# Kernel optimization log

Hardware: AMD Instinct MI355X
Metric: run time of the kernel (lower is better)

The kernel has to match this reference:

```python
import jax, jax.numpy as jnp
import numpy as np

N_NODES = 100000
N_EDGES = 3200000
IN_DIM = 128
HID = 64
OUT_DIM = 1


def gcn_conv(x, src, dst, W, b, n_nodes):
    # PyG GCNConv: h = X W; out = D^{-1/2} (A+I) D^{-1/2} h + b
    # (src, dst already include self-loops)
    h = x @ W  # [N, F_out]
    ones = jnp.ones(src.shape[0], dtype=x.dtype)
    deg = jax.ops.segment_sum(ones, dst, num_segments=n_nodes)  # in-degree with self-loops
    dinv = jnp.where(deg > 0, jax.lax.rsqrt(deg), 0.0)
    norm = dinv[src] * dinv[dst]  # [E]
    msg = h[src] * norm[:, None]  # [E, F_out] gather + scale
    agg = jax.ops.segment_sum(msg, dst, num_segments=n_nodes)  # scatter-add
    return agg + b


def setup_inputs() -> dict:
    key = jax.random.key(0)
    k = jax.random.split(key, 8)
    x = jax.random.normal(k[0], (N_NODES, IN_DIM), dtype=jnp.float32)
    edge_index = jax.random.randint(k[1], (2, N_EDGES), 0, N_NODES, dtype=jnp.int32)
    # Glorot-ish init for weights
    W1 = jax.random.normal(k[2], (IN_DIM, HID), dtype=jnp.float32) / np.sqrt(IN_DIM)
    b1 = jnp.zeros((HID,), dtype=jnp.float32)
    W2 = jax.random.normal(k[3], (HID, HID), dtype=jnp.float32) / np.sqrt(HID)
    b2 = jnp.zeros((HID,), dtype=jnp.float32)
    Wfc = jax.random.normal(k[4], (HID, OUT_DIM), dtype=jnp.float32) / np.sqrt(HID)
    bfc = jnp.zeros((OUT_DIM,), dtype=jnp.float32)
    return {"x": x, "edge_index": edge_index, "W1": W1, "b1": b1,
            "W2": W2, "b2": b2, "Wfc": Wfc, "bfc": bfc}


def reference(x, edge_index, W1, b1, W2, b2, Wfc, bfc):
    n = x.shape[0]
    loops = jnp.arange(n, dtype=edge_index.dtype)
    src = jnp.concatenate([edge_index[0], loops])
    dst = jnp.concatenate([edge_index[1], loops])
    h = jax.nn.relu(gcn_conv(x, src, dst, W1, b1, n))
    # dropout p=0.2 is identity in eval mode
    h = jax.nn.relu(gcn_conv(h, src, dst, W2, b2, n))
    out = h @ Wfc + bfc
    return jax.nn.sigmoid(out)
```

## Files before the change

### kernel.cpp

```cpp
#include <hip/hip_runtime.h>

#define INDIM 128
#define HIDD 64
#define BSHIFT 6
#define BNODES 64
#define BCAP 4096
#define MAXBUCK 2048
#define CHUNK 8192
#define ATHREADS 512
#define BPT (MAXBUCK / ATHREADS)

typedef float f32x2 __attribute__((ext_vector_type(2)));
typedef uint4 __attribute__((aligned(4))) uint4a;

__device__ inline unsigned short f2bf(float f) {
    unsigned u = __float_as_uint(f);
    return (unsigned short)((u + 0x7fff + ((u >> 16) & 1)) >> 16);
}
__device__ inline float bflo(unsigned v) { return __uint_as_float(v << 16); }


__global__ void k_zero(int* __restrict__ p, int n) {
    int i = blockIdx.x * blockDim.x + threadIdx.x;
    if (i < n) p[i] = 0;
}

__global__ __launch_bounds__(ATHREADS) void k_bucketA(
        const int* __restrict__ srcA, const int* __restrict__ dstA,
        int* __restrict__ bcnt, unsigned* __restrict__ bucketBuf,
        int E, int N, int NBUCK) {
    __shared__ int cnt[MAXBUCK];
    __shared__ int cur[MAXBUCK];
    __shared__ unsigned short gbase[MAXBUCK];
    __shared__ unsigned short stage[CHUNK];
    __shared__ int dLds[CHUNK];
    __shared__ int wsum[ATHREADS / 64];
    int t = threadIdx.x;
    int EV = E + N;
    int begin = blockIdx.x * CHUNK;
    int end = begin + CHUNK;
    if (end > EV) end = EV;
    if (begin >= EV) return;
    int nLoc = end - begin;

    for (int b = t; b < MAXBUCK; b += ATHREADS) cnt[b] = 0;
    __syncthreads();

    for (int i = begin + t; i < end; i += ATHREADS) {
        int d = (i < E) ? dstA[i] : (i - E);
        dLds[i - begin] = d;
        atomicAdd(&cnt[d >> BSHIFT], 1);
    }
    __syncthreads();

    int vq[BPT];
    int psum = 0;
#pragma unroll
    for (int q = 0; q < BPT; ++q) { vq[q] = cnt[t * BPT + q]; psum += vq[q]; }
    int lane = t & 63, w = t >> 6;
    int s = psum;
#pragma unroll
    for (int off = 1; off < 64; off <<= 1) {
        int u = __shfl_up(s, off, 64);
        if (lane >= off) s += u;
    }
    if (lane == 63) wsum[w] = s;
    __syncthreads();
    if (t < ATHREADS / 64) {
        int x = wsum[t];
#pragma unroll
        for (int off = 1; off < ATHREADS / 64; off <<= 1) {
            int u = __shfl_up(x, off, 64);
            if (t >= off) x += u;
        }
        wsum[t] = x;
    }
    __syncthreads();
    int run = ((w > 0) ? wsum[w - 1] : 0) + s - psum;
#pragma unroll
    for (int q = 0; q < BPT; ++q) {
        cur[t * BPT + q] = run;
        run += vq[q];
    }

    int b0 = (int)(((unsigned)blockIdx.x * 683u) % (unsigned)NBUCK);
    for (int idx = t; idx < NBUCK; idx += ATHREADS) {
        int b = idx + b0;
        if (b >= NBUCK) b -= NBUCK;
        int c = cnt[b];
        gbase[b] = (unsigned short)((c > 0) ? atomicAdd(&bcnt[b], c) : 0);
    }
    __syncthreads();

    for (int j = t; j < nLoc; j += ATHREADS) {
        int d = dLds[j];
        int slot = atomicAdd(&cur[d >> BSHIFT], 1);
        stage[slot] = (unsigned short)j;
    }
    __syncthreads();

    for (int j = t; j < nLoc; j += ATHREADS) {
        int loc = (int)stage[j];
        int d = dLds[loc];
        int i2 = begin + loc;
        int s2 = (i2 < E) ? srcA[i2] : d;
        int b = d >> BSHIFT;
        int local = j - (cur[b] - cnt[b]);
        int slot = (int)gbase[b] + local;
        if (slot < BCAP)
            bucketBuf[(size_t)b * BCAP + slot] = ((unsigned)s2 << BSHIFT) | (d & (BNODES - 1));
    }
}

__global__ __launch_bounds__(512) void k_scanbuck(const int* __restrict__ bcnt,
                                                  int* __restrict__ bstart,
                                                  int* __restrict__ rowStartN,
                                                  int NBUCK) {
    __shared__ int wsum[8];
    int t = threadIdx.x;
    int v[4];
    int psum = 0;
#pragma unroll
    for (int q = 0; q < 4; ++q) {
        int b = t * 4 + q;
        v[q] = (b < NBUCK) ? bcnt[b] : 0;
        psum += v[q];
    }
    int lane = t & 63, w = t >> 6;
    int s = psum;
#pragma unroll
    for (int off = 1; off < 64; off <<= 1) {
        int u = __shfl_up(s, off, 64);
        if (lane >= off) s += u;
    }
    if (lane == 63) wsum[w] = s;
    __syncthreads();
    if (t < 8) {
        int x = wsum[t];
#pragma unroll
        for (int off = 1; off < 8; off <<= 1) {
            int u = __shfl_up(x, off, 64);
            if (t >= off) x += u;
        }
        wsum[t] = x;
    }
    __syncthreads();
    int run = ((w > 0) ? wsum[w - 1] : 0) + s - psum;
#pragma unroll
    for (int q = 0; q < 4; ++q) {
        int b = t * 4 + q;
        if (b < NBUCK) bstart[b] = run;
        run += v[q];
    }
    if (t == 511) *rowStartN = run;
}

__global__ __launch_bounds__(256) void k_fillB(
        const int* __restrict__ bcnt, const unsigned* __restrict__ bucketBuf,
        const int* __restrict__ bstart, int* __restrict__ rowStart,
        float* __restrict__ dinv, int* __restrict__ srcList, int N) {
    __shared__ int cnt[BNODES];
    __shared__ int cur[BNODES];
    __shared__ unsigned stage[BCAP];
    int b = blockIdx.x;
    int t = threadIdx.x;
    if (t < BNODES) cnt[t] = 0;
    __syncthreads();
    int n = bcnt[b];
    if (n > BCAP) n = BCAP;
    int base = bstart[b];
    const unsigned* buf = bucketBuf + (size_t)b * BCAP;
    for (int e = t; e < n; e += 256)
        atomicAdd(&cnt[buf[e] & (BNODES - 1)], 1);
    __syncthreads();
    if (t < BNODES) {
        int c = cnt[t];
        int s = c;
#pragma unroll
        for (int off = 1; off < BNODES; off <<= 1) {
            int u = __shfl_up(s, off, 64);
            if (t >= off) s += u;
        }
        int excl = s - c;
        cur[t] = excl;
        int node = b * BNODES + t;
        if (node < N) {
            rowStart[node] = base + excl;
            dinv[node] = rsqrtf((float)c);
        }
    }
    __syncthreads();
    for (int e = t; e < n; e += 256) {
        unsigned entry = buf[e];
        int slot = atomicAdd(&cur[entry & (BNODES - 1)], 1);
        stage[slot] = entry;
    }
    __syncthreads();
    for (int j = t; j < n; j += 256)
        srcList[base + j] = (int)(stage[j] >> BSHIFT);
}

template <int K, bool BF16IN>
__global__ __launch_bounds__(256) void k_gemm_t(const void* __restrict__ Xv,
                                                const float* __restrict__ W,
                                                const float* __restrict__ dinv,
                                                unsigned short* __restrict__ Hs, int N) {
    __shared__ float Xs[64][68];
    __shared__ float Ws[64][64];
    int t = threadIdx.x;
    if (!BF16IN && blockIdx.x == 0 && t < 32)
        ((unsigned*)Hs)[(size_t)N * 32 + t] = 0u;
    int row0 = blockIdx.x * 64;
    int tr = t >> 4;
    int tc = t & 15;
    float acc[4][4] = {{0.f}};

    for (int kb = 0; kb < K; kb += 64) {
        if (!BF16IN) {
            const float* X = (const float*)Xv;
#pragma unroll
            for (int q = 0; q < 4; ++q) {
                int f = q * 256 + t;
                int r = f >> 4;
                int c4 = (f & 15) << 2;
                float4 v = make_float4(0.f, 0.f, 0.f, 0.f);
                int row = row0 + r;
                if (row < N) v = *(const float4*)&X[(size_t)row * K + kb + c4];
                *(float4*)&Xs[r][c4] = v;
            }
        } else {
            const unsigned* X = (const unsigned*)Xv;
#pragma unroll
            for (int q = 0; q < 4; ++q) {
                int f = q * 256 + t;
                int r = f >> 4;
                int c4 = (f & 15) << 2;
                int row = row0 + r;
                uint2 v = make_uint2(0u, 0u);
                if (row < N) v = *(const uint2*)&X[(size_t)row * 32 + (c4 >> 1)];
                Xs[r][c4 + 0] = bflo(v.x); Xs[r][c4 + 1] = __uint_as_float(v.x & 0xffff0000u);
                Xs[r][c4 + 2] = bflo(v.y); Xs[r][c4 + 3] = __uint_as_float(v.y & 0xffff0000u);
            }
        }
#pragma unroll
        for (int q = 0; q < 4; ++q) {
            int f = q * 256 + t;
            int kk = f >> 4;
            int c4 = (f & 15) << 2;
            *(float4*)&Ws[kk][c4] = *(const float4*)&W[(size_t)(kb + kk) * 64 + c4];
        }
        __syncthreads();

        for (int k = 0; k < 64; k += 4) {
            float4 xv0 = *(const float4*)&Xs[4 * tr + 0][k];
            float4 xv1 = *(const float4*)&Xs[4 * tr + 1][k];
            float4 xv2 = *(const float4*)&Xs[4 * tr + 2][k];
            float4 xv3 = *(const float4*)&Xs[4 * tr + 3][k];
            float4 wv0 = *(const float4*)&Ws[k + 0][4 * tc];
            float4 wv1 = *(const float4*)&Ws[k + 1][4 * tc];
            float4 wv2 = *(const float4*)&Ws[k + 2][4 * tc];
            float4 wv3 = *(const float4*)&Ws[k + 3][4 * tc];
            const float* xr[4] = {(const float*)&xv0, (const float*)&xv1,
                                  (const float*)&xv2, (const float*)&xv3};
            const float* wr[4] = {(const float*)&wv0, (const float*)&wv1,
                                  (const float*)&wv2, (const float*)&wv3};
#pragma unroll
            for (int kk = 0; kk < 4; ++kk)
#pragma unroll
                for (int i = 0; i < 4; ++i)
#pragma unroll
                    for (int c = 0; c < 4; ++c)
                        acc[i][c] += xr[i][kk] * wr[kk][c];
        }
        __syncthreads();
    }

#pragma unroll
    for (int i = 0; i < 4; ++i) {
        int row = row0 + 4 * tr + i;
        if (row < N) {
            float di = dinv[row];
            ushort4 o;
            o.x = f2bf(acc[i][0] * di);
            o.y = f2bf(acc[i][1] * di);
            o.z = f2bf(acc[i][2] * di);
            o.w = f2bf(acc[i][3] * di);
            *(ushort4*)&Hs[(size_t)row * HIDD + 4 * tc] = o;
        }
    }
}


#define PK2(accH, accL, u0, u1)                                              \
    do {                                                                     \
        f32x2 hh_, ll_;                                                      \
        hh_.x = __uint_as_float(u0);                                         \
        hh_.y = __uint_as_float(u1);                                         \
        ll_.x = __uint_as_float((u0) << 16);                                 \
        ll_.y = __uint_as_float((u1) << 16);                                 \
        asm("v_pk_add_f32 %0, %1, %0" : "+v"(accH) : "v"(hh_));              \
        asm("v_pk_add_f32 %0, %1, %0" : "+v"(accL) : "v"(ll_));              \
    } while (0)

#define ACC8R(v4)                                                            \
    do { PK2(h0, l0, (v4).x, (v4).y); PK2(h1, l1, (v4).z, (v4).w); } while (0)

#define ROW(sidx) (*(const uint4*)(Hb + (((unsigned)(sidx) << 7) + qb)))

#define AGG_BODY(HPTR)                                                       \
    const char* Hb = (const char*)(HPTR);                                    \
    unsigned qb = (unsigned)q << 4;                                          \
    int beg = rowStart[i], end = rowStart[i + 1];                            \
    f32x2 h0 = {0.f, 0.f}, l0 = {0.f, 0.f};                                  \
    f32x2 h1 = {0.f, 0.f}, l1 = {0.f, 0.f};                                  \
    int e = beg;                                                             \
    while (end - e > 48) {                            \
        uint4a sv = *(const uint4a*)&srcList[e + 4 * g];                     \
        uint4 v0 = ROW(sv.x);                                                \
        uint4 v1 = ROW(sv.y);                                                \
        uint4 v2 = ROW(sv.z);                                                \
        uint4 v3 = ROW(sv.w);                                                \
        ACC8R(v0); ACC8R(v1); ACC8R(v2); ACC8R(v3);                          \
        e += 32;                                                             \
    }                                                                        \
    {                                                                        \
        int rem = end - e;                                        \
        int b0 = e + 4 * g;                                                  \
        uint4a sv = *(const uint4a*)&srcList[b0];                \
        int s0 = (b0 + 0 < end) ? (int)sv.x : N;                             \
        int s1 = (b0 + 1 < end) ? (int)sv.y : N;                             \
        int s2 = (b0 + 2 < end) ? (int)sv.z : N;                             \
        int s3 = (b0 + 3 < end) ? (int)sv.w : N;                             \
        uint4 v0 = ROW(s0);                                                  \
        uint4 v1 = ROW(s1);                                                  \
        uint4 v2 = ROW(s2);                                                  \
        uint4 v3 = ROW(s3);                                                  \
        ACC8R(v0); ACC8R(v1); ACC8R(v2); ACC8R(v3);                          \
        if (rem > 32) {                                                      \
            int i4 = e + 32 + g;                                             \
            int s4 = (i4 < end) ? srcList[i4] : N;                           \
            uint4 v4 = ROW(s4);                                              \
            ACC8R(v4);                                                       \
            if (rem > 40) {                                                  \
                int i5 = e + 40 + g;                                         \
                int s5 = (i5 < end) ? srcList[i5] : N;                       \
                uint4 v5 = ROW(s5);                                          \
                ACC8R(v5);                                                   \
            }                                                                \
        }                                                                    \
    }                                                                        \
    float v8[8] = {l0.x, h0.x, l0.y, h0.y, l1.x, h1.x, l1.y, h1.y};          \
    _Pragma("unroll")                                                        \
    for (int k = 0; k < 8; ++k) {                                            \
        v8[k] += __shfl_xor(v8[k], 8, 64);                                   \
        v8[k] += __shfl_xor(v8[k], 16, 64);                                  \
        v8[k] += __shfl_xor(v8[k], 32, 64);                                  \
    }

__global__ __launch_bounds__(256) void k_agg_relu(
        const unsigned* __restrict__ Hs, const float* __restrict__ dinv,
        const int* __restrict__ rowStart, const int* __restrict__ srcList,
        const float* __restrict__ bias, unsigned* __restrict__ O, int N) {
    int wid  = (blockIdx.x * blockDim.x + threadIdx.x) >> 6;
    int lane = threadIdx.x & 63;
    if (wid >= N) return;
    int i = __builtin_amdgcn_readfirstlane(wid);
    int g = lane >> 3;
    int q = lane & 7;
    AGG_BODY(Hs)
    if (g == 0) {
        float di = dinv[i];
        float4 ba = *(const float4*)&bias[q * 8];
        float4 bb = *(const float4*)&bias[q * 8 + 4];
        const float* bp = (const float*)&ba;
        const float* bq = (const float*)&bb;
        float r0 = fmaxf(di * v8[0] + bp[0], 0.f);
        float r1 = fmaxf(di * v8[1] + bp[1], 0.f);
        float r2 = fmaxf(di * v8[2] + bp[2], 0.f);
        float r3 = fmaxf(di * v8[3] + bp[3], 0.f);
        float r4 = fmaxf(di * v8[4] + bq[0], 0.f);
        float r5 = fmaxf(di * v8[5] + bq[1], 0.f);
        float r6 = fmaxf(di * v8[6] + bq[2], 0.f);
        float r7 = fmaxf(di * v8[7] + bq[3], 0.f);
        uint4 o;
        asm("v_cvt_pk_bf16_f32 %0, %1, %2" : "=v"(o.x) : "v"(r0), "v"(r1));
        asm("v_cvt_pk_bf16_f32 %0, %1, %2" : "=v"(o.y) : "v"(r2), "v"(r3));
        asm("v_cvt_pk_bf16_f32 %0, %1, %2" : "=v"(o.z) : "v"(r4), "v"(r5));
        asm("v_cvt_pk_bf16_f32 %0, %1, %2" : "=v"(o.w) : "v"(r6), "v"(r7));
        *(uint4*)(O + (size_t)i * 32 + q * 4) = o;
    }
}

__global__ __launch_bounds__(256) void k_agg_fc(
        const unsigned* __restrict__ Hs, const float* __restrict__ dinv,
        const int* __restrict__ rowStart, const int* __restrict__ srcList,
        const float* __restrict__ b2, const float* __restrict__ Wfc,
        const float* __restrict__ bfc, float* __restrict__ out, int N) {
    int wid  = (blockIdx.x * blockDim.x + threadIdx.x) >> 6;
    int lane = threadIdx.x & 63;
    if (wid >= N) return;
    int i = __builtin_amdgcn_readfirstlane(wid);
    int g = lane >> 3;
    int q = lane & 7;
    AGG_BODY(Hs)
    if (g == 0) {
        float di = dinv[i];
        float4 ba = *(const float4*)&b2[q * 8];
        float4 bb = *(const float4*)&b2[q * 8 + 4];
        float4 wa = *(const float4*)&Wfc[q * 8];
        float4 wb = *(const float4*)&Wfc[q * 8 + 4];
        const float* bp = (const float*)&ba;
        const float* bq = (const float*)&bb;
        const float* wp = (const float*)&wa;
        const float* wq = (const float*)&wb;
        float p = 0.f;
#pragma unroll
        for (int k = 0; k < 4; ++k) p += fmaxf(di * v8[k] + bp[k], 0.f) * wp[k];
#pragma unroll
        for (int k = 0; k < 4; ++k) p += fmaxf(di * v8[4 + k] + bq[k], 0.f) * wq[k];
        p += __shfl_xor(p, 1, 64);
        p += __shfl_xor(p, 2, 64);
        p += __shfl_xor(p, 4, 64);
        if (q == 0) {
            float z = p + bfc[0];
            out[i] = 1.f / (1.f + __expf(-z));
        }
    }
}


extern "C" void kernel_launch(void* const* d_in, const int* in_sizes, int n_in,
                              void* d_out, int out_size, void* d_ws, size_t ws_size,
                              hipStream_t stream) {
    const float* x   = (const float*)d_in[0];
    const int*   ei  = (const int*)d_in[1];
    const float* W1  = (const float*)d_in[2];
    const float* b1  = (const float*)d_in[3];
    const float* W2  = (const float*)d_in[4];
    const float* b2  = (const float*)d_in[5];
    const float* Wfc = (const float*)d_in[6];
    const float* bfc = (const float*)d_in[7];
    float* out = (float*)d_out;

    int N  = in_sizes[0] / INDIM;
    int E  = in_sizes[1] / 2;
    int EV = E + N;
    const int* srcA = ei;
    const int* dstA = ei + E;

    int NBUCK = (N + BNODES - 1) / BNODES;
    size_t bucketBytes = (size_t)NBUCK * BCAP * 4;
    size_t hsBytes     = (size_t)(N + 1) * HIDD * 2;

    char* ws = (char*)d_ws;
    size_t off = 0;
    auto alloc = [&](size_t bytes) -> char* {
        char* p = ws + off;
        off = (off + bytes + 255) & ~(size_t)255;
        return p;
    };
    int*   rowStart = (int*)alloc((size_t)(N + 1) * 4);
    float* dinv     = (float*)alloc((size_t)N * 4);
    int*   bcnt     = (int*)alloc((size_t)NBUCK * 4);
    int*   bstart   = (int*)alloc((size_t)NBUCK * 4);
    int*   srcList  = (int*)alloc((size_t)(EV + 48) * 4);
    char*  region   = alloc(bucketBytes > hsBytes ? bucketBytes : hsBytes);
    unsigned*       bucketBuf = (unsigned*)region;
    unsigned short* Hs        = (unsigned short*)region;
    unsigned* bufB = (unsigned*)alloc(hsBytes);

    hipLaunchKernelGGL(k_zero, dim3((NBUCK + 255) / 256), dim3(256), 0, stream, bcnt, NBUCK);
    int aBlocks = (EV + CHUNK - 1) / CHUNK;
    hipLaunchKernelGGL(k_bucketA, dim3(aBlocks), dim3(ATHREADS), 0, stream,
                       srcA, dstA, bcnt, bucketBuf, E, N, NBUCK);
    hipLaunchKernelGGL(k_scanbuck, dim3(1), dim3(512), 0, stream,
                       bcnt, bstart, rowStart + N, NBUCK);
    hipLaunchKernelGGL(k_fillB, dim3(NBUCK), dim3(256), 0, stream,
                       bcnt, bucketBuf, bstart, rowStart, dinv, srcList, N);

    int gBlocks = (N + 63) / 64;
    hipLaunchKernelGGL((k_gemm_t<INDIM, false>), dim3(gBlocks), dim3(256), 0, stream,
                       (const void*)x, W1, dinv, Hs, N);

    int aggBlocks = (N + 3) / 4;
    hipLaunchKernelGGL(k_agg_relu, dim3(aggBlocks), dim3(256), 0, stream,
                       (const unsigned*)Hs, dinv, rowStart, srcList, b1, bufB, N);

    hipLaunchKernelGGL((k_gemm_t<HIDD, true>), dim3(gBlocks), dim3(256), 0, stream,
                       (const void*)bufB, W2, dinv, Hs, N);

    hipLaunchKernelGGL(k_agg_fc, dim3(aggBlocks), dim3(256), 0, stream,
                       (const unsigned*)Hs, dinv, rowStart, srcList, b2, Wfc, bfc, out, N);
}
```

Measured before the change: 203.7 us.

## Use bf16 MFMA with hi/lo split for the dense GEMMs

Replaces the scalar fp32 LDS-tiled GEMM with a bf16 MFMA 16x16x32 kernel. To keep near-fp32 accuracy, it splits the fp32 inputs and weights into high and low bf16 parts and accumulates three products. The aggregation loop now loads source indices as scalar strided reads instead of unaligned uint4 reads. The bucket-counter zeroing kernel is replaced with hipMemsetAsync. Risks are slightly different rounding, extra conversion work, and narrower 2-byte output stores.

```diff
diff --git a/kernel.cpp b/kernel.cpp
--- a/kernel.cpp
+++ b/kernel.cpp
@@ -11,19 +11,20 @@
 #define BPT (MAXBUCK / ATHREADS)
 
 typedef float f32x2 __attribute__((ext_vector_type(2)));
-typedef uint4 __attribute__((aligned(4))) uint4a;
+using short8 = __attribute__((ext_vector_type(8))) short;
+using f32x4  = __attribute__((ext_vector_type(4))) float;
 
 __device__ inline unsigned short f2bf(float f) {
     unsigned u = __float_as_uint(f);
     return (unsigned short)((u + 0x7fff + ((u >> 16) & 1)) >> 16);
 }
 __device__ inline float bflo(unsigned v) { return __uint_as_float(v << 16); }
-
-
-__global__ void k_zero(int* __restrict__ p, int n) {
-    int i = blockIdx.x * blockDim.x + threadIdx.x;
-    if (i < n) p[i] = 0;
-}
+__device__ inline unsigned cvtpk(float a, float b) {
+    unsigned r;
+    asm("v_cvt_pk_bf16_f32 %0, %1, %2" : "=v"(r) : "v"(a), "v"(b));
+    return r;
+}
+
 
 __global__ __launch_bounds__(ATHREADS) void k_bucketA(
         const int* __restrict__ srcA, const int* __restrict__ dstA,
@@ -200,92 +201,104 @@
         srcList[base + j] = (int)(stage[j] >> BSHIFT);
 }
 
-template <int K, bool BF16IN>
-__global__ __launch_bounds__(256) void k_gemm_t(const void* __restrict__ Xv,
-                                                const float* __restrict__ W,
-                                                const float* __restrict__ dinv,
-                                                unsigned short* __restrict__ Hs, int N) {
-    __shared__ float Xs[64][68];
-    __shared__ float Ws[64][64];
+template <int K, bool F32IN>
+__global__ __launch_bounds__(256) void k_gemm_mfma(const void* __restrict__ Xv,
+                                                   const float* __restrict__ W,
+                                                   const float* __restrict__ dinv,
+                                                   unsigned short* __restrict__ Hs,
+                                                   int N) {
+    __shared__ unsigned short AH[64][72];
+    __shared__ unsigned short AL[64][72];
+    __shared__ unsigned short BH[64][72];
+    __shared__ unsigned short BL[64][72];
     int t = threadIdx.x;
-    if (!BF16IN && blockIdx.x == 0 && t < 32)
+    int row0 = blockIdx.x * 64;
+    if (F32IN && blockIdx.x == 0 && t < 32)
         ((unsigned*)Hs)[(size_t)N * 32 + t] = 0u;
-    int row0 = blockIdx.x * 64;
-    int tr = t >> 4;
-    int tc = t & 15;
-    float acc[4][4] = {{0.f}};
+    int w = t >> 6, lane = t & 63;
+    int lr = lane & 15, lh = lane >> 4;
+    f32x4 acc[4];
+#pragma unroll
+    for (int tn = 0; tn < 4; ++tn) acc[tn] = (f32x4){0.f, 0.f, 0.f, 0.f};
 
     for (int kb = 0; kb < K; kb += 64) {
-        if (!BF16IN) {
+        if (kb) __syncthreads();
+        if constexpr (F32IN) {
             const float* X = (const float*)Xv;
 #pragma unroll
-            for (int q = 0; q < 4; ++q) {
-                int f = q * 256 + t;
-                int r = f >> 4;
-                int c4 = (f & 15) << 2;
-                float4 v = make_float4(0.f, 0.f, 0.f, 0.f);
+            for (int qq = 0; qq < 4; ++qq) {
+                int f = qq * 256 + t;
+                int r = f >> 4, c4 = (f & 15) << 2;
                 int row = row0 + r;
-                if (row < N) v = *(const float4*)&X[(size_t)row * K + kb + c4];
-                *(float4*)&Xs[r][c4] = v;
+                float4 x = make_float4(0.f, 0.f, 0.f, 0.f);
+                if (row < N) x = *(const float4*)&X[(size_t)row * K + kb + c4];
+                unsigned u01 = cvtpk(x.x, x.y), u23 = cvtpk(x.z, x.w);
+                float l0 = x.x - bflo(u01);
+                float l1 = x.y - __uint_as_float(u01 & 0xffff0000u);
+                float l2 = x.z - bflo(u23);
+                float l3 = x.w - __uint_as_float(u23 & 0xffff0000u);
+                unsigned v01 = cvtpk(l0, l1), v23 = cvtpk(l2, l3);
+                *(uint2*)&AH[r][c4] = make_uint2(u01, u23);
+                *(uint2*)&AL[r][c4] = make_uint2(v01, v23);
             }
         } else {
             const unsigned* X = (const unsigned*)Xv;
 #pragma unroll
-            for (int q = 0; q < 4; ++q) {
-                int f = q * 256 + t;
-                int r = f >> 4;
-                int c4 = (f & 15) << 2;
+            for (int qq = 0; qq < 2; ++qq) {
+                int f = qq * 256 + t;
+                int r = f >> 3, c8 = (f & 7) << 3;
                 int row = row0 + r;
-                uint2 v = make_uint2(0u, 0u);
-                if (row < N) v = *(const uint2*)&X[(size_t)row * 32 + (c4 >> 1)];
-                Xs[r][c4 + 0] = bflo(v.x); Xs[r][c4 + 1] = __uint_as_float(v.x & 0xffff0000u);
-                Xs[r][c4 + 2] = bflo(v.y); Xs[r][c4 + 3] = __uint_as_float(v.y & 0xffff0000u);
+                uint4 v = make_uint4(0u, 0u, 0u, 0u);
+                if (row < N) v = *(const uint4*)&X[(size_t)row * 32 + (c8 >> 1)];
+                *(uint4*)&AH[r][c8] = v;
             }
         }
-#pragma unroll
-        for (int q = 0; q < 4; ++q) {
-            int f = q * 256 + t;
-            int kk = f >> 4;
-            int c4 = (f & 15) << 2;
-            *(float4*)&Ws[kk][c4] = *(const float4*)&W[(size_t)(kb + kk) * 64 + c4];
+        {
+            int n = (t & 15) + ((t >> 6) << 4);
+            int kc0 = ((t >> 4) & 3) << 2;
+#pragma unroll
+            for (int qq = 0; qq < 4; ++qq) {
+                int kc = kc0 + (qq << 4);
+                float w0 = W[(size_t)(kb + kc + 0) * HIDD + n];
+                float w1 = W[(size_t)(kb + kc + 1) * HIDD + n];
+                float w2 = W[(size_t)(kb + kc + 2) * HIDD + n];
+                float w3 = W[(size_t)(kb + kc + 3) * HIDD + n];
+                unsigned u01 = cvtpk(w0, w1), u23 = cvtpk(w2, w3);
+                float l0 = w0 - bflo(u01);
+                float l1 = w1 - __uint_as_float(u01 & 0xffff0000u);
+                float l2 = w2 - bflo(u23);
+                float l3 = w3 - __uint_as_float(u23 & 0xffff0000u);
+                unsigned v01 = cvtpk(l0, l1), v23 = cvtpk(l2, l3);
+                *(uint2*)&BH[n][kc] = make_uint2(u01, u23);
+                *(uint2*)&BL[n][kc] = make_uint2(v01, v23);
+            }
         }
         __syncthreads();
-
-        for (int k = 0; k < 64; k += 4) {
-            float4 xv0 = *(const float4*)&Xs[4 * tr + 0][k];
-            float4 xv1 = *(const float4*)&Xs[4 * tr + 1][k];
-            float4 xv2 = *(const float4*)&Xs[4 * tr + 2][k];
-            float4 xv3 = *(const float4*)&Xs[4 * tr + 3][k];
-            float4 wv0 = *(const float4*)&Ws[k + 0][4 * tc];
-            float4 wv1 = *(const float4*)&Ws[k + 1][4 * tc];
-            float4 wv2 = *(const float4*)&Ws[k + 2][4 * tc];
-            float4 wv3 = *(const float4*)&Ws[k + 3][4 * tc];
-            const float* xr[4] = {(const float*)&xv0, (const float*)&xv1,
-                                  (const float*)&xv2, (const float*)&xv3};
-            const float* wr[4] = {(const float*)&wv0, (const float*)&wv1,
-                                  (const float*)&wv2, (const float*)&wv3};
-#pragma unroll
-            for (int kk = 0; kk < 4; ++kk)
-#pragma unroll
-                for (int i = 0; i < 4; ++i)
-#pragma unroll
-                    for (int c = 0; c < 4; ++c)
-                        acc[i][c] += xr[i][kk] * wr[kk][c];
-        }
-        __syncthreads();
-    }
-
-#pragma unroll
-    for (int i = 0; i < 4; ++i) {
-        int row = row0 + 4 * tr + i;
+#pragma unroll
+        for (int s = 0; s < 2; ++s) {
+            short8 ah = *(const short8*)&AH[16 * w + lr][32 * s + 8 * lh];
+#pragma unroll
+            for (int tn = 0; tn < 4; ++tn) {
+                short8 bh = *(const short8*)&BH[16 * tn + lr][32 * s + 8 * lh];
+                short8 bl = *(const short8*)&BL[16 * tn + lr][32 * s + 8 * lh];
+                acc[tn] = __builtin_amdgcn_mfma_f32_16x16x32_bf16(ah, bh, acc[tn], 0, 0, 0);
+                acc[tn] = __builtin_amdgcn_mfma_f32_16x16x32_bf16(ah, bl, acc[tn], 0, 0, 0);
+                if constexpr (F32IN) {
+                    short8 al = *(const short8*)&AL[16 * w + lr][32 * s + 8 * lh];
+                    acc[tn] = __builtin_amdgcn_mfma_f32_16x16x32_bf16(al, bh, acc[tn], 0, 0, 0);
+                }
+            }
+        }
+    }
+    int rb = row0 + 16 * w + 4 * lh;
+#pragma unroll
+    for (int r = 0; r < 4; ++r) {
+        int row = rb + r;
         if (row < N) {
             float di = dinv[row];
-            ushort4 o;
-            o.x = f2bf(acc[i][0] * di);
-            o.y = f2bf(acc[i][1] * di);
-            o.z = f2bf(acc[i][2] * di);
-            o.w = f2bf(acc[i][3] * di);
-            *(ushort4*)&Hs[(size_t)row * HIDD + 4 * tc] = o;
+#pragma unroll
+            for (int tn = 0; tn < 4; ++tn)
+                Hs[(size_t)row * HIDD + 16 * tn + lr] = f2bf(acc[tn][r] * di);
         }
     }
 }
@@ -305,7 +318,7 @@
 #define ACC8R(v4)                                                            \
     do { PK2(h0, l0, (v4).x, (v4).y); PK2(h1, l1, (v4).z, (v4).w); } while (0)
 
-#define ROW(sidx) (*(const uint4*)(Hb + (((unsigned)(sidx) << 7) + qb)))
+#define ROWG(sidx) (*(const uint4*)(Hb + (((unsigned)(sidx) << 7) + qb)))
 
 #define AGG_BODY(HPTR)                                                       \
     const char* Hb = (const char*)(HPTR);                                    \
@@ -315,39 +328,33 @@
     f32x2 h1 = {0.f, 0.f}, l1 = {0.f, 0.f};                                  \
     int e = beg;                                                             \
     while (end - e > 48) {                            \
-        uint4a sv = *(const uint4a*)&srcList[e + 4 * g];                     \
-        uint4 v0 = ROW(sv.x);                                                \
-        uint4 v1 = ROW(sv.y);                                                \
-        uint4 v2 = ROW(sv.z);                                                \
-        uint4 v3 = ROW(sv.w);                                                \
+        int s0 = srcList[e + g];                                             \
+        int s1 = srcList[e + 8 + g];                                         \
+        int s2 = srcList[e + 16 + g];                                        \
+        int s3 = srcList[e + 24 + g];                                        \
+        uint4 v0 = ROWG(s0);                                                 \
+        uint4 v1 = ROWG(s1);                                                 \
+        uint4 v2 = ROWG(s2);                                                 \
+        uint4 v3 = ROWG(s3);                                                 \
         ACC8R(v0); ACC8R(v1); ACC8R(v2); ACC8R(v3);                          \
         e += 32;                                                             \
     }                                                                        \
     {                                                                        \
-        int rem = end - e;                                        \
-        int b0 = e + 4 * g;                                                  \
-        uint4a sv = *(const uint4a*)&srcList[b0];                \
-        int s0 = (b0 + 0 < end) ? (int)sv.x : N;                             \
-        int s1 = (b0 + 1 < end) ? (int)sv.y : N;                             \
-        int s2 = (b0 + 2 < end) ? (int)sv.z : N;                             \
-        int s3 = (b0 + 3 < end) ? (int)sv.w : N;                             \
-        uint4 v0 = ROW(s0);                                                  \
-        uint4 v1 = ROW(s1);                                                  \
-        uint4 v2 = ROW(s2);                                                  \
-        uint4 v3 = ROW(s3);                                                  \
-        ACC8R(v0); ACC8R(v1); ACC8R(v2); ACC8R(v3);                          \
-        if (rem > 32) {                                                      \
-            int i4 = e + 32 + g;                                             \
-            int s4 = (i4 < end) ? srcList[i4] : N;                           \
-            uint4 v4 = ROW(s4);                                              \
-            ACC8R(v4);                                                       \
-            if (rem > 40) {                                                  \
-                int i5 = e + 40 + g;                                         \
-                int s5 = (i5 < end) ? srcList[i5] : N;                       \
-                uint4 v5 = ROW(s5);                                          \
-                ACC8R(v5);                                                   \
-            }                                                                \
-        }                                                                    \
+        int i0 = e + g,      i1 = e + 8 + g,  i2 = e + 16 + g;               \
+        int i3 = e + 24 + g, i4 = e + 32 + g, i5 = e + 40 + g;               \
+        int s0 = (i0 < end) ? srcList[i0] : N;                               \
+        int s1 = (i1 < end) ? srcList[i1] : N;                               \
+        int s2 = (i2 < end) ? srcList[i2] : N;                               \
+        int s3 = (i3 < end) ? srcList[i3] : N;                               \
+        int s4 = (i4 < end) ? srcList[i4] : N;                               \
+        int s5 = (i5 < end) ? srcList[i5] : N;                               \
+        uint4 v0 = ROWG(s0);                                                 \
+        uint4 v1 = ROWG(s1);                                                 \
+        uint4 v2 = ROWG(s2);                                                 \
+        uint4 v3 = ROWG(s3);                                                 \
+        uint4 v4 = ROWG(s4);                                                 \
+        uint4 v5 = ROWG(s5);                                                 \
+        ACC8R(v0); ACC8R(v1); ACC8R(v2); ACC8R(v3); ACC8R(v4); ACC8R(v5);    \
     }                                                                        \
     float v8[8] = {l0.x, h0.x, l0.y, h0.y, l1.x, h1.x, l1.y, h1.y};          \
     _Pragma("unroll")                                                        \
@@ -383,10 +390,10 @@
         float r6 = fmaxf(di * v8[6] + bq[2], 0.f);
         float r7 = fmaxf(di * v8[7] + bq[3], 0.f);
         uint4 o;
-        asm("v_cvt_pk_bf16_f32 %0, %1, %2" : "=v"(o.x) : "v"(r0), "v"(r1));
-        asm("v_cvt_pk_bf16_f32 %0, %1, %2" : "=v"(o.y) : "v"(r2), "v"(r3));
-        asm("v_cvt_pk_bf16_f32 %0, %1, %2" : "=v"(o.z) : "v"(r4), "v"(r5));
-        asm("v_cvt_pk_bf16_f32 %0, %1, %2" : "=v"(o.w) : "v"(r6), "v"(r7));
+        o.x = cvtpk(r0, r1);
+        o.y = cvtpk(r2, r3);
+        o.z = cvtpk(r4, r5);
+        o.w = cvtpk(r6, r7);
         *(uint4*)(O + (size_t)i * 32 + q * 4) = o;
     }
 }
@@ -469,7 +476,7 @@
     unsigned short* Hs        = (unsigned short*)region;
     unsigned* bufB = (unsigned*)alloc(hsBytes);
 
-    hipLaunchKernelGGL(k_zero, dim3((NBUCK + 255) / 256), dim3(256), 0, stream, bcnt, NBUCK);
+    hipMemsetAsync(bcnt, 0, (size_t)NBUCK * 4, stream);
     int aBlocks = (EV + CHUNK - 1) / CHUNK;
     hipLaunchKernelGGL(k_bucketA, dim3(aBlocks), dim3(ATHREADS), 0, stream,
                        srcA, dstA, bcnt, bucketBuf, E, N, NBUCK);
@@ -479,14 +486,14 @@
                        bcnt, bucketBuf, bstart, rowStart, dinv, srcList, N);
 
     int gBlocks = (N + 63) / 64;
-    hipLaunchKernelGGL((k_gemm_t<INDIM, false>), dim3(gBlocks), dim3(256), 0, stream,
+    hipLaunchKernelGGL((k_gemm_mfma<INDIM, true>), dim3(gBlocks), dim3(256), 0, stream,
                        (const void*)x, W1, dinv, Hs, N);
 
     int aggBlocks = (N + 3) / 4;
     hipLaunchKernelGGL(k_agg_relu, dim3(aggBlocks), dim3(256), 0, stream,
                        (const unsigned*)Hs, dinv, rowStart, srcList, b1, bufB, N);
 
-    hipLaunchKernelGGL((k_gemm_t<HIDD, true>), dim3(gBlocks), dim3(256), 0, stream,
+    hipLaunchKernelGGL((k_gemm_mfma<HIDD, false>), dim3(gBlocks), dim3(256), 0, stream,
                        (const void*)bufB, W2, dinv, Hs, N);
 
     hipLaunchKernelGGL(k_agg_fc, dim3(aggBlocks), dim3(256), 0, stream,
```

Result: faster. 177.9 us (-12.6%).
